# Optimization experiments

Hardware: AMD Instinct MI355X
Metric: run time of the kernel (lower is better)

## Reference

```python
import jax, jax.numpy as jnp
import numpy as np

HID = 2048
NKH, NVH = 16, 32
DK, DV = 128, 128
KCONV = 4
KEY_DIM = NKH * DK          # 2048
VAL_DIM = NVH * DV          # 4096
CONV_DIM = 2 * KEY_DIM + VAL_DIM  # 8192
QKVZ_DIM = 2 * KEY_DIM + 2 * VAL_DIM  # 12288
R = NVH // NKH              # 2
BA_DIM = 2 * NVH            # 64
EPS = 1e-6


def _l2norm(x, eps=1e-6):
    return x * jax.lax.rsqrt(jnp.sum(x * x, axis=-1, keepdims=True) + eps)


def setup_inputs() -> dict:
    key = jax.random.key(0)
    ks = jax.random.split(key, 8)
    std = 0.02
    return {
        "hidden_states": jax.random.normal(ks[0], (2, 2048, HID), dtype=jnp.float32),
        "attention_mask": jnp.ones((2, 2048), dtype=jnp.float32),
        "W_qkvz": jax.random.normal(ks[1], (HID, QKVZ_DIM), dtype=jnp.float32) * std,
        "W_ba": jax.random.normal(ks[2], (HID, BA_DIM), dtype=jnp.float32) * std,
        "conv_kernel": jax.random.normal(ks[3], (KCONV, 1, CONV_DIM), dtype=jnp.float32) * 0.1,
        "A_log": jnp.log(jax.random.uniform(ks[4], (NVH,), dtype=jnp.float32, minval=1.0, maxval=16.0)),
        "dt_bias": jnp.ones((NVH,), dtype=jnp.float32),
        "norm_kernel": jnp.ones((DV,), dtype=jnp.float32),
        "W_out": jax.random.normal(ks[5], (VAL_DIM, HID), dtype=jnp.float32) * std,
    }


def reference(hidden_states, attention_mask, W_qkvz, W_ba, conv_kernel, A_log, dt_bias, norm_kernel, W_out):
    b, s, _ = hidden_states.shape
    h = hidden_states * attention_mask[:, :, None]  # apply padding mask

    # projections
    qkvz = h @ W_qkvz  # (b, s, QKVZ_DIM)
    ba = h @ W_ba      # (b, s, BA_DIM)

    # fix_query_key_value_ordering: grouped per-k-head layout [q, k, v*R, z*R]
    qkvz = qkvz.reshape(b, s, NKH, 2 * DK + 2 * R * DV)
    q = qkvz[..., :DK]                                   # (b,s,NKH,DK)
    k = qkvz[..., DK:2 * DK]                             # (b,s,NKH,DK)
    v = qkvz[..., 2 * DK:2 * DK + R * DV].reshape(b, s, NVH, DV)
    z = qkvz[..., 2 * DK + R * DV:].reshape(b, s, NVH, DV)
    ba = ba.reshape(b, s, NKH, 2 * R)
    beta = ba[..., :R].reshape(b, s, NVH)
    alpha = ba[..., R:].reshape(b, s, NVH)

    # causal depthwise conv over [q|k|v] channels
    conv_in = jnp.concatenate(
        [q.reshape(b, s, -1), k.reshape(b, s, -1), v.reshape(b, s, -1)], axis=-1)  # (b,s,CONV_DIM)
    conv_out = jax.lax.conv_general_dilated(
        conv_in, conv_kernel, window_strides=(1,), padding=((KCONV - 1, 0),),
        dimension_numbers=("NWC", "WIO", "NWC"), feature_group_count=CONV_DIM)
    conv_out = jax.nn.silu(conv_out)

    q = conv_out[..., :KEY_DIM].reshape(b, s, NKH, DK)
    k = conv_out[..., KEY_DIM:2 * KEY_DIM].reshape(b, s, NKH, DK)
    v = conv_out[..., 2 * KEY_DIM:].reshape(b, s, NVH, DV)

    # expand k-heads to v-heads (repeat_interleave)
    q = jnp.repeat(q, R, axis=2)  # (b,s,NVH,DK)
    k = jnp.repeat(k, R, axis=2)

    # gated delta rule parameters
    g = -jnp.exp(A_log)[None, None, :] * jax.nn.softplus(alpha + dt_bias[None, None, :])  # (b,s,NVH)
    beta = jax.nn.sigmoid(beta)
    q = _l2norm(q) * (DK ** -0.5)
    k = _l2norm(k)

    # recurrence: S_t = exp(g_t) * S_{t-1} + k_t (v_t - k_t^T S) beta_t ; o_t = q_t^T S_t
    def step(S, x):
        q_t, k_t, v_t, g_t, b_t = x
        S = S * jnp.exp(g_t)[..., None, None]               # (b,h,DK,DV)
        kv = jnp.einsum("bhk,bhkv->bhv", k_t, S)
        delta = (v_t - kv) * b_t[..., None]
        S = S + jnp.einsum("bhk,bhv->bhkv", k_t, delta)
        o_t = jnp.einsum("bhk,bhkv->bhv", q_t, S)
        return S, o_t

    xs = (q.transpose(1, 0, 2, 3), k.transpose(1, 0, 2, 3), v.transpose(1, 0, 2, 3),
          g.transpose(1, 0, 2), beta.transpose(1, 0, 2))
    S0 = jnp.zeros((b, NVH, DK, DV), dtype=hidden_states.dtype)
    _, o = jax.lax.scan(step, S0, xs)
    o = o.transpose(1, 0, 2, 3)  # (b,s,NVH,DV)

    # gated RMSNorm per head (fp32 math as in Qwen3NextRMSNormGated)
    of = o.astype(jnp.float32)
    var = jnp.mean(of * of, axis=-1, keepdims=True)
    of = of * jax.lax.rsqrt(var + EPS)
    of = norm_kernel * of
    of = of * jax.nn.silu(z.astype(jnp.float32))
    o = of.astype(o.dtype).reshape(b, s, VAL_DIM)

    return o @ W_out
```

## Files before the change

kernel.cpp:

```cpp
#include <hip/hip_runtime.h>
#include <stdint.h>

typedef float    f32x4 __attribute__((ext_vector_type(4)));
typedef float    f32x2 __attribute__((ext_vector_type(2)));
typedef _Float16 f16x8 __attribute__((ext_vector_type(8)));
typedef _Float16 f16x4 __attribute__((ext_vector_type(4)));
typedef _Float16 f16x2 __attribute__((ext_vector_type(2)));

#define SEQ   2048
#define HIDD  2048
#define MROWS 4096
#define NQKV  12288
#define NCHUNK 32
#define CLEN   64

__device__ __forceinline__ void gload_lds16(const void* g, void* l) {
  __builtin_amdgcn_global_load_lds((const __attribute__((address_space(1))) uint32_t*)g,
                                   (__attribute__((address_space(3))) uint32_t*)l, 16, 0, 0);
}
__device__ __forceinline__ int swz256(int row, int colb) { return row * 256 + (colb ^ ((row & 7) << 4)); }
__device__ __forceinline__ int swz128(int row, int colb) { return row * 128 + (colb ^ ((row & 7) << 4)); }

__global__ __launch_bounds__(256)
void amask_kernel(const float* __restrict__ h, const float* __restrict__ mask,
                  _Float16* __restrict__ A1) {
  int i = blockIdx.x * 256 + threadIdx.x;
  if (i >= MROWS * HIDD / 4) return;
  f32x4 x = ((const f32x4*)h)[i];
  float m = mask[(i * 4) >> 11];
  f16x4 r;
  r[0] = (_Float16)(x[0] * m); r[1] = (_Float16)(x[1] * m);
  r[2] = (_Float16)(x[2] * m); r[3] = (_Float16)(x[3] * m);
  *(f16x4*)(A1 + (size_t)i * 4) = r;
}

__global__ __launch_bounds__(256)
void transpose_f16(const float* __restrict__ in, _Float16* __restrict__ out,
                   int R, int C) {
  __shared__ float tile[64][65];
  int c0 = blockIdx.x * 64, r0 = blockIdx.y * 64;
  int tx = threadIdx.x & 63, ty = threadIdx.x >> 6;
  #pragma unroll
  for (int i = 0; i < 16; ++i) {
    int r = i * 4 + ty;
    tile[r][tx] = in[(size_t)(r0 + r) * C + c0 + tx];
  }
  __syncthreads();
  #pragma unroll
  for (int i = 0; i < 16; ++i) {
    int c = i * 4 + ty;
    out[(size_t)(c0 + c) * R + r0 + tx] = (_Float16)tile[tx][c];
  }
}

template <typename CT, int BM>
__global__ __launch_bounds__(512, 2)
void gemm2ph(const _Float16* __restrict__ A, const _Float16* __restrict__ Bt,
             CT* __restrict__ C, int M, int N, int K, int tiles_n) {
  constexpr int RF  = BM / 32;
  constexpr int AR  = BM / 8;
  constexpr int NA  = AR / 8;
  constexpr int STG = NA + 4;
  __shared__ __align__(16) _Float16 lsA[2][BM * 64];
  __shared__ __align__(16) _Float16 lsB[2][256 * 64];
  int bm = blockIdx.x / tiles_n, bn = blockIdx.x % tiles_n;
  int m0 = bm * BM, n0 = bn * 256;
  int tid = threadIdx.x;
  int w = tid >> 6, lane = tid & 63;
  int wm = w >> 2, wn = w & 3;
  int la = lane & 15, lk = lane >> 4;
  int sr = lane >> 3;
  int scb = ((lane & 7) << 4) ^ ((sr & 7) << 4);
  int nkt = K >> 6;
  f32x4 acc[RF][4] = {};

  auto stage = [&](int kt, int buf) {
    const char* ga = (const char*)(A  + (size_t)(m0 + w * AR) * K + kt * 64);
    const char* gb = (const char*)(Bt + (size_t)(n0 + w * 32) * K + kt * 64);
    #pragma unroll
    for (int i = 0; i < NA; ++i)
      gload_lds16(ga + (size_t)(i * 8 + sr) * (K * 2) + scb, &lsA[buf][(w * AR + i * 8) * 64]);
    #pragma unroll
    for (int i = 0; i < 4; ++i)
      gload_lds16(gb + (size_t)(i * 8 + sr) * (K * 2) + scb, &lsB[buf][(w * 32 + i * 8) * 64]);
  };

  stage(0, 0);
  if (nkt > 1) stage(1, 1);

  int cur = 0;
  for (int kt = 0; kt < nkt; ++kt) {
    if (kt < nkt - 1) asm volatile("s_waitcnt vmcnt(%0)" :: "i"(STG) : "memory");
    else              asm volatile("s_waitcnt vmcnt(0)" ::: "memory");
    __builtin_amdgcn_s_barrier();
    const char* cA = (const char*)&lsA[cur][0];
    const char* cB = (const char*)&lsB[cur][0];
    #pragma unroll
    for (int kw = 0; kw < 2; ++kw) {
      f16x8 af[RF], bf[4];
      #pragma unroll
      for (int f = 0; f < RF; ++f) {
        int row = wm * (BM / 2) + f * 16 + la;
        af[f] = *(const f16x8*)(cA + row * 128 + ((kw * 64 + lk * 16) ^ ((row & 7) << 4)));
      }
      #pragma unroll
      for (int j = 0; j < 4; ++j) {
        int row = wn * 64 + j * 16 + la;
        bf[j] = *(const f16x8*)(cB + row * 128 + ((kw * 64 + lk * 16) ^ ((row & 7) << 4)));
      }
      #pragma unroll
      for (int f = 0; f < RF; ++f)
        #pragma unroll
        for (int j = 0; j < 4; ++j)
          acc[f][j] = __builtin_amdgcn_mfma_f32_16x16x32_f16(af[f], bf[j], acc[f][j], 0, 0, 0);
    }
    __builtin_amdgcn_s_barrier();
    if (kt + 2 < nkt) stage(kt + 2, cur);
    cur ^= 1;
  }

  #pragma unroll
  for (int f = 0; f < RF; ++f)
    #pragma unroll
    for (int j = 0; j < 4; ++j) {
      int col = n0 + wn * 64 + j * 16 + la;
      #pragma unroll
      for (int r = 0; r < 4; ++r) {
        int row = m0 + wm * (BM / 2) + f * 16 + lk * 4 + r;
        C[(size_t)row * N + col] = (CT)acc[f][j][r];
      }
    }
}

__global__ __launch_bounds__(256)
void ba_gemm(const float* __restrict__ h, const float* __restrict__ mask,
             const float* __restrict__ Wba, float* __restrict__ ba) {
  __shared__ float red[4][8][64];
  int r0 = blockIdx.x * 8;
  int c = threadIdx.x & 63, kc = threadIdx.x >> 6;
  float acc[8] = {};
  const float* wp = Wba + (size_t)(kc * 512) * 64 + c;
  const float* hp = h + (size_t)r0 * HIDD + kc * 512;
  for (int i = 0; i < 512; ++i) {
    float w = wp[(size_t)i * 64];
    #pragma unroll
    for (int r = 0; r < 8; ++r)
      acc[r] += hp[(size_t)r * HIDD + i] * w;
  }
  #pragma unroll
  for (int r = 0; r < 8; ++r) red[kc][r][c] = acc[r];
  __syncthreads();
  if (kc == 0) {
    #pragma unroll
    for (int r = 0; r < 8; ++r) {
      float s = red[0][r][c] + red[1][r][c] + red[2][r][c] + red[3][r][c];
      ba[(size_t)(r0 + r) * 64 + c] = s * mask[r0 + r];
    }
  }
}

__global__ __launch_bounds__(256)
void conv_kernel(const _Float16* __restrict__ qkvz, const float* __restrict__ ck,
                 _Float16* __restrict__ qn, _Float16* __restrict__ kn,
                 _Float16* __restrict__ vb) {
  int row = blockIdx.x;
  int b = row >> 11, t = row & 2047;
  int lane = threadIdx.x & 63, wid = threadIdx.x >> 6;
  for (int u = wid; u < 64; u += 4) {
    int c, cc, hh;
    if (u < 16)      { hh = u;      c = hh * 768;                               cc = hh * 128; }
    else if (u < 32) { hh = u - 16; c = hh * 768 + 128;                         cc = 2048 + hh * 128; }
    else             { hh = u - 32; c = (hh >> 1) * 768 + 256 + (hh & 1) * 128; cc = 4096 + hh * 128; }
    float y0 = 0.f, y1 = 0.f;
    #pragma unroll
    for (int j = 0; j < 4; ++j) {
      int tt = t - 3 + j;
      if (tt >= 0) {
        const _Float16* r = qkvz + (size_t)(b * 2048 + tt) * NQKV + c;
        f16x2 x = *(const f16x2*)(r + 2 * lane);
        f32x2 w = *(const f32x2*)(ck + j * 8192 + cc + 2 * lane);
        y0 += (float)x[0] * w[0];
        y1 += (float)x[1] * w[1];
      }
    }
    y0 = y0 / (1.f + expf(-y0));
    y1 = y1 / (1.f + expf(-y1));
    if (u < 32) {
      float ss = y0 * y0 + y1 * y1;
      #pragma unroll
      for (int m = 1; m < 64; m <<= 1) ss += __shfl_xor(ss, m);
      float rs = rsqrtf(ss + 1e-6f);
      if (u < 16) rs *= 0.08838834764831845f;
      y0 *= rs; y1 *= rs;
      _Float16* dst = (u < 16 ? qn : kn) + (size_t)row * 2048 + hh * 128;
      f16x2 o; o[0] = (_Float16)y0; o[1] = (_Float16)y1;
      *(f16x2*)(dst + 2 * lane) = o;
    } else {
      _Float16* dst = vb + (size_t)row * 4096 + hh * 128;
      f16x2 o; o[0] = (_Float16)y0; o[1] = (_Float16)y1;
      *(f16x2*)(dst + 2 * lane) = o;
    }
  }
}

__global__ __launch_bounds__(256)
void egbeta_kernel(const float* __restrict__ ba, const float* __restrict__ Alog,
                   const float* __restrict__ dtb, float* __restrict__ gout,
                   float* __restrict__ bout) {
  int i = blockIdx.x * 256 + threadIdx.x;
  if (i >= MROWS * 32) return;
  int vh = i >> 12, row = i & 4095;
  int kh = vh >> 1, r = vh & 1;
  const float* p = ba + (size_t)row * 64 + kh * 4;
  float bv = p[r], av = p[2 + r];
  float x = av + dtb[vh];
  float sp = (x > 20.f) ? x : log1pf(expf(x));
  gout[(size_t)vh * MROWS + row] = -expf(Alog[vh]) * sp;
  bout[(size_t)vh * MROWS + row] = 1.f / (1.f + expf(-bv));
}

__global__ __launch_bounds__(512, 2)
void chunk_scan(const _Float16* __restrict__ qn, const _Float16* __restrict__ kn,
                _Float16* __restrict__ vb, const float* __restrict__ gb,
                const float* __restrict__ btb) {
  __shared__ __align__(16) _Float16 Ks[64 * 128];
  __shared__ __align__(16) _Float16 Qs[64 * 128];
  __shared__ __align__(16) _Float16 Kt[128 * 64];
  __shared__ __align__(16) _Float16 Sf[32 * 128];
  __shared__ float AT[64 * 65];
  __shared__ __align__(16) _Float16 M16[64 * 64];
  __shared__ float RHS[32 * 65];
  __shared__ __align__(16) _Float16 Uv[32 * 64];
  __shared__ __align__(16) _Float16 Ub[32 * 64];
  __shared__ __align__(16) _Float16 Vb[64 * 32];
  __shared__ float gs[64], bs[64], cgs[64], bexp[64], scU[64];

  char* Ksb = (char*)Ks; char* Qsb = (char*)Qs; char* Ktb = (char*)Kt;
  char* Sfb = (char*)Sf; char* M16b = (char*)M16;
  char* Uvb = (char*)Uv; char* Ubb = (char*)Ub; char* Vbb = (char*)Vb;

  int bid = blockIdx.x;
  int b = bid >> 7, vh = (bid >> 2) & 31, vsl = bid & 3;
  int kh = vh >> 1;
  int tid = threadIdx.x;
  int w = tid >> 6, lane = tid & 63;
  int wr = w >> 1, wc = w & 1;
  int la = lane & 15, lk = lane >> 4;

  const _Float16* kgb = kn + (size_t)(b * 2048) * 2048 + kh * 128;
  const _Float16* qgb = qn + (size_t)(b * 2048) * 2048 + kh * 128;
  _Float16*       vgb = vb + (size_t)(b * 2048) * 4096 + vh * 128 + vsl * 32;
  const float*    ggb = gb  + (size_t)vh * MROWS + b * 2048;
  const float*    bgb = btb + (size_t)vh * MROWS + b * 2048;

  int srow = tid >> 3, sseg = tid & 7;
  int tk = tid & 127, tth = tid >> 7;

  f16x8 kr[2], qr[2]; f16x4 vr; float ebr;
  float sreg[2][4] = {};

  { f32x4 z = {}; ((f32x4*)Sf)[tid] = z; }

  kr[0] = *(const f16x8*)(kgb + (size_t)srow * 2048 + sseg * 16);
  kr[1] = *(const f16x8*)(kgb + (size_t)srow * 2048 + sseg * 16 + 8);
  qr[0] = *(const f16x8*)(qgb + (size_t)srow * 2048 + sseg * 16);
  qr[1] = *(const f16x8*)(qgb + (size_t)srow * 2048 + sseg * 16 + 8);
  vr    = *(const f16x4*)(vgb + (size_t)srow * 4096 + sseg * 4);
  ebr   = (tid < 64) ? ggb[tid] : (tid < 128 ? bgb[tid - 64] : 0.f);
  *(f16x8*)(Ksb + swz256(srow, sseg * 32))      = kr[0];
  *(f16x8*)(Ksb + swz256(srow, sseg * 32 + 16)) = kr[1];
  *(f16x8*)(Qsb + swz256(srow, sseg * 32))      = qr[0];
  *(f16x8*)(Qsb + swz256(srow, sseg * 32 + 16)) = qr[1];
  *(f16x4*)(Vbb + srow * 64 + sseg * 8) = vr;
  if (tid < 64) gs[tid] = ebr; else if (tid < 128) bs[tid - 64] = ebr;
  __syncthreads();

  #pragma unroll 1
  for (int c = 0; c < NCHUNK; ++c) {
    int cn = (c < NCHUNK - 1) ? c + 1 : c;
    kr[0] = *(const f16x8*)(kgb + (size_t)(cn * 64 + srow) * 2048 + sseg * 16);
    kr[1] = *(const f16x8*)(kgb + (size_t)(cn * 64 + srow) * 2048 + sseg * 16 + 8);
    qr[0] = *(const f16x8*)(qgb + (size_t)(cn * 64 + srow) * 2048 + sseg * 16);
    qr[1] = *(const f16x8*)(qgb + (size_t)(cn * 64 + srow) * 2048 + sseg * 16 + 8);
    vr    = *(const f16x4*)(vgb + (size_t)(cn * 64 + srow) * 4096 + sseg * 4);
    ebr   = (tid < 64) ? ggb[cn * 64 + tid] : (tid < 128 ? bgb[cn * 64 + tid - 64] : 0.f);

    f32x4 kk[2] = {}, qk[2] = {}, ks0 = {}, qs0 = {};
    #pragma unroll
    for (int ks = 0; ks < 4; ++ks) {
      f16x8 aK = *(const f16x8*)(Ksb + swz256(wr * 16 + la, ks * 64 + lk * 16));
      f16x8 aQ = *(const f16x8*)(Qsb + swz256(wr * 16 + la, ks * 64 + lk * 16));
      f16x8 bS = *(const f16x8*)(Sfb + swz256(wc * 16 + la, ks * 64 + lk * 16));
      #pragma unroll
      for (int j = 0; j < 2; ++j) {
        f16x8 bK = *(const f16x8*)(Ksb + swz256(wc * 32 + j * 16 + la, ks * 64 + lk * 16));
        kk[j] = __builtin_amdgcn_mfma_f32_16x16x32_f16(aK, bK, kk[j], 0, 0, 0);
        qk[j] = __builtin_amdgcn_mfma_f32_16x16x32_f16(aQ, bK, qk[j], 0, 0, 0);
      }
      ks0 = __builtin_amdgcn_mfma_f32_16x16x32_f16(aK, bS, ks0, 0, 0, 0);
      qs0 = __builtin_amdgcn_mfma_f32_16x16x32_f16(aQ, bS, qs0, 0, 0, 0);
    }
    {
      f16x8 r0, r1;
      #pragma unroll
      for (int j = 0; j < 8; ++j) {
        r0[j] = *(const _Float16*)(Ksb + swz256(tth * 16 + j, 2 * tk));
        r1[j] = *(const _Float16*)(Ksb + swz256(tth * 16 + 8 + j, 2 * tk));
      }
      *(f16x8*)(Ktb + swz128(tk, tth * 32))      = r0;
      *(f16x8*)(Ktb + swz128(tk, tth * 32 + 16)) = r1;
    }
    if (w == 0) {
      float g = gs[lane];
      #pragma unroll
      for (int off = 1; off < 64; off <<= 1) {
        float y = __shfl_up(g, off);
        if (lane >= off) g += y;
      }
      cgs[lane] = g;
      float cgL = __shfl(g, 63);
      bexp[lane] = __expf(g);
      scU[lane] = bs[lane] * __expf(cgL - g);
    }
    __syncthreads();

    {
      float cgt[4];
      #pragma unroll
      for (int r = 0; r < 4; ++r) cgt[r] = cgs[wr * 16 + lk * 4 + r];
      #pragma unroll
      for (int j = 0; j < 2; ++j) {
        int s = wc * 32 + j * 16 + la;
        float bsv = bs[s], cgss = cgs[s];
        #pragma unroll
        for (int r = 0; r < 4; ++r) {
          int t = wr * 16 + lk * 4 + r;
          float e = bsv * __expf(cgt[r] - cgss);
          AT[s * 65 + t] = (s < t) ? e * kk[j][r] : 0.f;
          float mm = (s <= t) ? e * qk[j][r] : 0.f;
          *(_Float16*)(M16b + swz128(t, s * 2)) = (_Float16)mm;
        }
      }
      #pragma unroll
      for (int r = 0; r < 4; ++r) {
        int t = wr * 16 + lk * 4 + r;
        int v = wc * 16 + la;
        float be = bexp[t];
        qs0[r] *= be;
        float vv = (float)*(const _Float16*)(Vbb + t * 64 + v * 2);
        RHS[v * 65 + t] = vv - be * ks0[r];
      }
    }
    __syncthreads();

    {
      float u[4];
      #pragma unroll
      for (int vi = 0; vi < 4; ++vi) u[vi] = RHS[(w * 4 + vi) * 65 + lane];
      #pragma unroll 1
      for (int sb = 0; sb < 8; ++sb) {
        float Ac[8];
        #pragma unroll
        for (int j = 0; j < 8; ++j) Ac[j] = AT[(sb * 8 + j) * 65 + lane];
        #pragma unroll
        for (int j = 0; j < 8; ++j) {
          int s = sb * 8 + j;
          #pragma unroll
          for (int vi = 0; vi < 4; ++vi) {
            float ubv = __builtin_bit_cast(float,
                __builtin_amdgcn_readlane(__builtin_bit_cast(int, u[vi]), s));
            u[vi] = fmaf(-Ac[j], ubv, u[vi]);
          }
        }
      }
      float sc = scU[lane];
      #pragma unroll
      for (int vi = 0; vi < 4; ++vi) {
        int v = w * 4 + vi;
        *(_Float16*)(Uvb + swz128(v, lane * 2)) = (_Float16)u[vi];
        *(_Float16*)(Ubb + swz128(v, lane * 2)) = (_Float16)(u[vi] * sc);
      }
    }
    __syncthreads();

    #pragma unroll
    for (int ss = 0; ss < 2; ++ss) {
      f16x8 aM = *(const f16x8*)(M16b + swz128(wr * 16 + la, ss * 64 + lk * 16));
      f16x8 bU = *(const f16x8*)(Uvb + swz128(wc * 16 + la, ss * 64 + lk * 16));
      qs0 = __builtin_amdgcn_mfma_f32_16x16x32_f16(aM, bU, qs0, 0, 0, 0);
    }
    #pragma unroll
    for (int r = 0; r < 4; ++r) {
      int t = wr * 16 + lk * 4 + r;
      vgb[(size_t)(c * 64 + t) * 4096 + wc * 16 + la] = (_Float16)qs0[r];
    }
    {
      f32x4 sd[2] = {};
      #pragma unroll
      for (int ss = 0; ss < 2; ++ss) {
        f16x8 bK = *(const f16x8*)(Ktb + swz128(w * 16 + la, ss * 64 + lk * 16));
        #pragma unroll
        for (int vt = 0; vt < 2; ++vt) {
          f16x8 aU = *(const f16x8*)(Ubb + swz128(vt * 16 + la, ss * 64 + lk * 16));
          sd[vt] = __builtin_amdgcn_mfma_f32_16x16x32_f16(aU, bK, sd[vt], 0, 0, 0);
        }
      }
      float beC = bexp[63];
      #pragma unroll
      for (int vt = 0; vt < 2; ++vt)
        #pragma unroll
        for (int r = 0; r < 4; ++r) {
          int v = vt * 16 + lk * 4 + r;
          int k = w * 16 + la;
          float sn = fmaf(sreg[vt][r], beC, sd[vt][r]);
          sreg[vt][r] = sn;
          *(_Float16*)(Sfb + swz256(v, k * 2)) = (_Float16)sn;
        }
    }
    __syncthreads();

    *(f16x8*)(Ksb + swz256(srow, sseg * 32))      = kr[0];
    *(f16x8*)(Ksb + swz256(srow, sseg * 32 + 16)) = kr[1];
    *(f16x8*)(Qsb + swz256(srow, sseg * 32))      = qr[0];
    *(f16x8*)(Qsb + swz256(srow, sseg * 32 + 16)) = qr[1];
    *(f16x4*)(Vbb + srow * 64 + sseg * 8) = vr;
    if (tid < 64) gs[tid] = ebr; else if (tid < 128) bs[tid - 64] = ebr;
    __syncthreads();
  }
}

__global__ __launch_bounds__(256)
void gate_kernel(const _Float16* __restrict__ ob, const _Float16* __restrict__ qkvz,
                 const float* __restrict__ nk, _Float16* __restrict__ Ag) {
  int row = blockIdx.x;
  int lane = threadIdx.x & 63, wid = threadIdx.x >> 6;
  for (int vh = wid; vh < 32; vh += 4) {
    const _Float16* op = ob + (size_t)row * 4096 + vh * 128;
    f16x2 xx = *(const f16x2*)(op + 2 * lane);
    float x0 = (float)xx[0], x1 = (float)xx[1];
    float ss = x0 * x0 + x1 * x1;
    #pragma unroll
    for (int m = 1; m < 64; m <<= 1) ss += __shfl_xor(ss, m);
    float rs = rsqrtf(ss * (1.f / 128.f) + 1e-6f);
    f32x2 nv = *(const f32x2*)(nk + 2 * lane);
    float v0 = x0 * rs * nv[0], v1 = x1 * rs * nv[1];
    const _Float16* zp = qkvz + (size_t)row * NQKV + (vh >> 1) * 768 + 512 + (vh & 1) * 128;
    f16x2 zz = *(const f16x2*)(zp + 2 * lane);
    float z0 = (float)zz[0], z1 = (float)zz[1];
    v0 *= z0 / (1.f + expf(-z0));
    v1 *= z1 / (1.f + expf(-z1));
    _Float16* dst = Ag + (size_t)row * 4096 + vh * 128;
    f16x2 o; o[0] = (_Float16)v0; o[1] = (_Float16)v1;
    *(f16x2*)(dst + 2 * lane) = o;
  }
}

extern "C" void kernel_launch(void* const* d_in, const int* in_sizes, int n_in,
                              void* d_out, int out_size, void* d_ws, size_t ws_size,
                              hipStream_t stream) {
  const float* h     = (const float*)d_in[0];
  const float* mask  = (const float*)d_in[1];
  const float* Wqkvz = (const float*)d_in[2];
  const float* Wba   = (const float*)d_in[3];
  const float* ck    = (const float*)d_in[4];
  const float* Alog  = (const float*)d_in[5];
  const float* dtb   = (const float*)d_in[6];
  const float* nk    = (const float*)d_in[7];
  const float* Wout  = (const float*)d_in[8];
  float* out = (float*)d_out;

  char* w = (char*)d_ws;
  const size_t o_qkvz = 0;
  const size_t o_A1   = 100663296;
  const size_t o_Bt1  = o_A1 + 16777216;
  const size_t o_ba   = o_Bt1 + 50331648;
  const size_t o_g    = o_ba + 1048576;
  const size_t o_bt   = o_g + 524288;
  const size_t total  = o_bt + 524288;
  if (ws_size < total) return;

  _Float16* qkvz16 = (_Float16*)(w + o_qkvz);
  _Float16* A1     = (_Float16*)(w + o_A1);
  _Float16* Bt1    = (_Float16*)(w + o_Bt1);
  float*    ba32   = (float*)   (w + o_ba);
  float*    gbuf   = (float*)   (w + o_g);
  float*    btb    = (float*)   (w + o_bt);
  _Float16* qn16 = (_Float16*)(w + o_A1);
  _Float16* kn16 = (_Float16*)(w + o_Bt1);
  _Float16* vb16 = (_Float16*)(w + o_Bt1 + 16777216);
  _Float16* Ag   = (_Float16*)(w + o_A1);
  _Float16* Wt2  = (_Float16*)(w + 0);

  amask_kernel<<<MROWS * HIDD / 4 / 256, 256, 0, stream>>>(h, mask, A1);
  transpose_f16<<<dim3(192, 32), 256, 0, stream>>>(Wqkvz, Bt1, HIDD, NQKV);
  ba_gemm<<<MROWS / 8, 256, 0, stream>>>(h, mask, Wba, ba32);
  gemm2ph<_Float16, 256><<<16 * 48, 512, 0, stream>>>(A1, Bt1, qkvz16, MROWS, NQKV, HIDD, 48);
  conv_kernel<<<MROWS, 256, 0, stream>>>(qkvz16, ck, qn16, kn16, vb16);
  egbeta_kernel<<<MROWS * 32 / 256, 256, 0, stream>>>(ba32, Alog, dtb, gbuf, btb);
  chunk_scan<<<256, 512, 0, stream>>>(qn16, kn16, vb16, gbuf, btb);
  gate_kernel<<<MROWS, 256, 0, stream>>>(vb16, qkvz16, nk, Ag);
  transpose_f16<<<dim3(32, 64), 256, 0, stream>>>(Wout, Wt2, 4096, HIDD);
  gemm2ph<float, 128><<<32 * 8, 512, 0, stream>>>(Ag, Wt2, out, MROWS, HIDD, 4096, 8);
}
```

Measured before the change: 700.2 us.

## Restructure GEMM main loop into barrier-separated phases with priority-boosted MFMA bursts

The GEMM k-loop now has a single-stage-ahead prefetch instead of prefetching two tiles. Each iteration loads B fragments and half of the A fragments into registers, then issues the next tile's global-to-LDS load. It runs four MFMA sub-phases separated by workgroup barriers, using s_setprio to raise priority during MFMA bursts and sched_barrier to pin instruction order. The intent is to overlap global loads with MFMA work and to interleave the two co-resident waves on each SIMD, in the style of 8-wave ping-pong schedules. The cost is many more barriers per iteration and a full vmcnt(0) wait at the top of every iteration, which could expose load latency.

```diff
diff --git a/kernel.cpp b/kernel.cpp
--- a/kernel.cpp
+++ b/kernel.cpp
@@ -55,12 +55,12 @@
 
 template <typename CT, int BM>
 __global__ __launch_bounds__(512, 2)
-void gemm2ph(const _Float16* __restrict__ A, const _Float16* __restrict__ Bt,
-             CT* __restrict__ C, int M, int N, int K, int tiles_n) {
+void gemm8p(const _Float16* __restrict__ A, const _Float16* __restrict__ Bt,
+            CT* __restrict__ C, int M, int N, int K, int tiles_n) {
   constexpr int RF  = BM / 32;
+  constexpr int RH  = RF / 2;
   constexpr int AR  = BM / 8;
   constexpr int NA  = AR / 8;
-  constexpr int STG = NA + 4;
   __shared__ __align__(16) _Float16 lsA[2][BM * 64];
   __shared__ __align__(16) _Float16 lsB[2][256 * 64];
   int bm = blockIdx.x / tiles_n, bn = blockIdx.x % tiles_n;
@@ -86,36 +86,85 @@
   };
 
   stage(0, 0);
-  if (nkt > 1) stage(1, 1);
 
   int cur = 0;
   for (int kt = 0; kt < nkt; ++kt) {
-    if (kt < nkt - 1) asm volatile("s_waitcnt vmcnt(%0)" :: "i"(STG) : "memory");
-    else              asm volatile("s_waitcnt vmcnt(0)" ::: "memory");
-    __builtin_amdgcn_s_barrier();
+    asm volatile("s_waitcnt vmcnt(0)" ::: "memory");
+    __builtin_amdgcn_s_barrier();
+    __builtin_amdgcn_sched_barrier(0);
     const char* cA = (const char*)&lsA[cur][0];
     const char* cB = (const char*)&lsB[cur][0];
-    #pragma unroll
-    for (int kw = 0; kw < 2; ++kw) {
-      f16x8 af[RF], bf[4];
-      #pragma unroll
-      for (int f = 0; f < RF; ++f) {
-        int row = wm * (BM / 2) + f * 16 + la;
-        af[f] = *(const f16x8*)(cA + row * 128 + ((kw * 64 + lk * 16) ^ ((row & 7) << 4)));
-      }
-      #pragma unroll
-      for (int j = 0; j < 4; ++j) {
+    f16x8 bf[4][2], af[RH][2];
+    #pragma unroll
+    for (int j = 0; j < 4; ++j)
+      #pragma unroll
+      for (int kw = 0; kw < 2; ++kw) {
         int row = wn * 64 + j * 16 + la;
-        bf[j] = *(const f16x8*)(cB + row * 128 + ((kw * 64 + lk * 16) ^ ((row & 7) << 4)));
-      }
-      #pragma unroll
-      for (int f = 0; f < RF; ++f)
-        #pragma unroll
-        for (int j = 0; j < 4; ++j)
-          acc[f][j] = __builtin_amdgcn_mfma_f32_16x16x32_f16(af[f], bf[j], acc[f][j], 0, 0, 0);
-    }
-    __builtin_amdgcn_s_barrier();
-    if (kt + 2 < nkt) stage(kt + 2, cur);
+        bf[j][kw] = *(const f16x8*)(cB + row * 128 + ((kw * 64 + lk * 16) ^ ((row & 7) << 4)));
+      }
+    #pragma unroll
+    for (int r = 0; r < RH; ++r)
+      #pragma unroll
+      for (int kw = 0; kw < 2; ++kw) {
+        int row = wm * (BM / 2) + r * 16 + la;
+        af[r][kw] = *(const f16x8*)(cA + row * 128 + ((kw * 64 + lk * 16) ^ ((row & 7) << 4)));
+      }
+    if (kt + 1 < nkt) stage(kt + 1, cur ^ 1);
+    __builtin_amdgcn_s_barrier();
+    __builtin_amdgcn_sched_barrier(0);
+    __builtin_amdgcn_s_setprio(1);
+    #pragma unroll
+    for (int r = 0; r < RH; ++r)
+      #pragma unroll
+      for (int j = 0; j < 2; ++j)
+        #pragma unroll
+        for (int kw = 0; kw < 2; ++kw)
+          acc[r][j] = __builtin_amdgcn_mfma_f32_16x16x32_f16(af[r][kw], bf[j][kw], acc[r][j], 0, 0, 0);
+    __builtin_amdgcn_s_setprio(0);
+    __builtin_amdgcn_s_barrier();
+    __builtin_amdgcn_sched_barrier(0);
+    __builtin_amdgcn_s_setprio(1);
+    #pragma unroll
+    for (int r = 0; r < RH; ++r)
+      #pragma unroll
+      for (int j = 2; j < 4; ++j)
+        #pragma unroll
+        for (int kw = 0; kw < 2; ++kw)
+          acc[r][j] = __builtin_amdgcn_mfma_f32_16x16x32_f16(af[r][kw], bf[j][kw], acc[r][j], 0, 0, 0);
+    __builtin_amdgcn_s_setprio(0);
+    __builtin_amdgcn_s_barrier();
+    __builtin_amdgcn_sched_barrier(0);
+    #pragma unroll
+    for (int r = 0; r < RH; ++r)
+      #pragma unroll
+      for (int kw = 0; kw < 2; ++kw) {
+        int row = wm * (BM / 2) + (RH + r) * 16 + la;
+        af[r][kw] = *(const f16x8*)(cA + row * 128 + ((kw * 64 + lk * 16) ^ ((row & 7) << 4)));
+      }
+    __builtin_amdgcn_s_barrier();
+    __builtin_amdgcn_sched_barrier(0);
+    __builtin_amdgcn_s_setprio(1);
+    #pragma unroll
+    for (int r = 0; r < RH; ++r)
+      #pragma unroll
+      for (int j = 0; j < 2; ++j)
+        #pragma unroll
+        for (int kw = 0; kw < 2; ++kw)
+          acc[RH + r][j] = __builtin_amdgcn_mfma_f32_16x16x32_f16(af[r][kw], bf[j][kw], acc[RH + r][j], 0, 0, 0);
+    __builtin_amdgcn_s_setprio(0);
+    __builtin_amdgcn_s_barrier();
+    __builtin_amdgcn_sched_barrier(0);
+    __builtin_amdgcn_s_setprio(1);
+    #pragma unroll
+    for (int r = 0; r < RH; ++r)
+      #pragma unroll
+      for (int j = 2; j < 4; ++j)
+        #pragma unroll
+        for (int kw = 0; kw < 2; ++kw)
+          acc[RH + r][j] = __builtin_amdgcn_mfma_f32_16x16x32_f16(af[r][kw], bf[j][kw], acc[RH + r][j], 0, 0, 0);
+    __builtin_amdgcn_s_setprio(0);
+    __builtin_amdgcn_s_barrier();
+    __builtin_amdgcn_sched_barrier(0);
     cur ^= 1;
   }
 
@@ -494,11 +543,11 @@
   amask_kernel<<<MROWS * HIDD / 4 / 256, 256, 0, stream>>>(h, mask, A1);
   transpose_f16<<<dim3(192, 32), 256, 0, stream>>>(Wqkvz, Bt1, HIDD, NQKV);
   ba_gemm<<<MROWS / 8, 256, 0, stream>>>(h, mask, Wba, ba32);
-  gemm2ph<_Float16, 256><<<16 * 48, 512, 0, stream>>>(A1, Bt1, qkvz16, MROWS, NQKV, HIDD, 48);
+  gemm8p<_Float16, 256><<<16 * 48, 512, 0, stream>>>(A1, Bt1, qkvz16, MROWS, NQKV, HIDD, 48);
   conv_kernel<<<MROWS, 256, 0, stream>>>(qkvz16, ck, qn16, kn16, vb16);
   egbeta_kernel<<<MROWS * 32 / 256, 256, 0, stream>>>(ba32, Alog, dtb, gbuf, btb);
   chunk_scan<<<256, 512, 0, stream>>>(qn16, kn16, vb16, gbuf, btb);
   gate_kernel<<<MROWS, 256, 0, stream>>>(vb16, qkvz16, nk, Ag);
   transpose_f16<<<dim3(32, 64), 256, 0, stream>>>(Wout, Wt2, 4096, HIDD);
-  gemm2ph<float, 128><<<32 * 8, 512, 0, stream>>>(Ag, Wt2, out, MROWS, HIDD, 4096, 8);
-}
+  gemm8p<float, 128><<<32 * 8, 512, 0, stream>>>(Ag, Wt2, out, MROWS, HIDD, 4096, 8);
+}
```

New measurement: 693.6 us. About the same (-0.9%).

## Restructure GEMM main loop into barrier-separated read/MFMA phases with XCD tile remap

Applied to the files above, without the earlier changes.

Replaces the two-stage prefetch GEMM loop with a one-ahead prefetch issued right after the first LDS reads. Each k-tile becomes alternating phases of LDS fragment reads and MFMA bursts, separated by workgroup barriers and sched_barriers, with raised wave priority during MFMA. Block indices are remapped so consecutive tiles land on the same XCD, aiming for better L2 reuse. The aim is to overlap LDS reads and global loads with matrix math across the two resident waves per SIMD. The trade-off is more barriers per k-tile and a shallower prefetch distance, with a full vmcnt(0) wait at the top of each iteration.

```diff
diff --git a/kernel.cpp b/kernel.cpp
--- a/kernel.cpp
+++ b/kernel.cpp
@@ -53,17 +53,20 @@
   }
 }
 
+#define SCHED0() __builtin_amdgcn_sched_barrier(0)
 template <typename CT, int BM>
 __global__ __launch_bounds__(512, 2)
-void gemm2ph(const _Float16* __restrict__ A, const _Float16* __restrict__ Bt,
-             CT* __restrict__ C, int M, int N, int K, int tiles_n) {
+void gemm4p(const _Float16* __restrict__ A, const _Float16* __restrict__ Bt,
+            CT* __restrict__ C, int M, int N, int K, int tiles_n) {
   constexpr int RF  = BM / 32;
+  constexpr int RH  = RF / 2;
   constexpr int AR  = BM / 8;
   constexpr int NA  = AR / 8;
-  constexpr int STG = NA + 4;
   __shared__ __align__(16) _Float16 lsA[2][BM * 64];
   __shared__ __align__(16) _Float16 lsB[2][256 * 64];
-  int bm = blockIdx.x / tiles_n, bn = blockIdx.x % tiles_n;
+  int cpx = gridDim.x >> 3;
+  int lid = (blockIdx.x & 7) * cpx + (blockIdx.x >> 3);
+  int bm = lid / tiles_n, bn = lid % tiles_n;
   int m0 = bm * BM, n0 = bn * 256;
   int tid = threadIdx.x;
   int w = tid >> 6, lane = tid & 63;
@@ -85,37 +88,49 @@
       gload_lds16(gb + (size_t)(i * 8 + sr) * (K * 2) + scb, &lsB[buf][(w * 32 + i * 8) * 64]);
   };
 
+#define READ_AF(dst, mh, kw)                                                       \
+  _Pragma("unroll") for (int r = 0; r < RH; ++r) {                                 \
+    int row_ = wm * (BM / 2) + ((mh) * RH + r) * 16 + la;                          \
+    dst[r] = *(const f16x8*)(cA + row_ * 128 + (((kw) * 64 + lk * 16) ^ ((row_ & 7) << 4))); }
+#define READ_BF(kw)                                                                \
+  _Pragma("unroll") for (int j = 0; j < 4; ++j) {                                  \
+    int row_ = wn * 64 + j * 16 + la;                                              \
+    bf[j] = *(const f16x8*)(cB + row_ * 128 + (((kw) * 64 + lk * 16) ^ ((row_ & 7) << 4))); }
+#define MFMA_PH(src, mh)                                                           \
+  __builtin_amdgcn_s_setprio(1);                                                   \
+  _Pragma("unroll") for (int r = 0; r < RH; ++r)                                   \
+    _Pragma("unroll") for (int j = 0; j < 4; ++j)                                  \
+      acc[(mh) * RH + r][j] =                                                      \
+        __builtin_amdgcn_mfma_f32_16x16x32_f16(src[r], bf[j], acc[(mh) * RH + r][j], 0, 0, 0); \
+  __builtin_amdgcn_s_setprio(0);
+
   stage(0, 0);
-  if (nkt > 1) stage(1, 1);
 
   int cur = 0;
   for (int kt = 0; kt < nkt; ++kt) {
-    if (kt < nkt - 1) asm volatile("s_waitcnt vmcnt(%0)" :: "i"(STG) : "memory");
-    else              asm volatile("s_waitcnt vmcnt(0)" ::: "memory");
+    asm volatile("s_waitcnt vmcnt(0)" ::: "memory");
     __builtin_amdgcn_s_barrier();
+    SCHED0();
     const char* cA = (const char*)&lsA[cur][0];
     const char* cB = (const char*)&lsB[cur][0];
-    #pragma unroll
-    for (int kw = 0; kw < 2; ++kw) {
-      f16x8 af[RF], bf[4];
-      #pragma unroll
-      for (int f = 0; f < RF; ++f) {
-        int row = wm * (BM / 2) + f * 16 + la;
-        af[f] = *(const f16x8*)(cA + row * 128 + ((kw * 64 + lk * 16) ^ ((row & 7) << 4)));
-      }
-      #pragma unroll
-      for (int j = 0; j < 4; ++j) {
-        int row = wn * 64 + j * 16 + la;
-        bf[j] = *(const f16x8*)(cB + row * 128 + ((kw * 64 + lk * 16) ^ ((row & 7) << 4)));
-      }
-      #pragma unroll
-      for (int f = 0; f < RF; ++f)
-        #pragma unroll
-        for (int j = 0; j < 4; ++j)
-          acc[f][j] = __builtin_amdgcn_mfma_f32_16x16x32_f16(af[f], bf[j], acc[f][j], 0, 0, 0);
-    }
-    __builtin_amdgcn_s_barrier();
-    if (kt + 2 < nkt) stage(kt + 2, cur);
+    f16x8 af0[RH], af1[RH], bf[4];
+    READ_BF(0); READ_AF(af0, 0, 0);
+    if (kt + 1 < nkt) stage(kt + 1, cur ^ 1);
+    SCHED0(); __builtin_amdgcn_s_barrier(); SCHED0();
+    MFMA_PH(af0, 0);
+    SCHED0(); __builtin_amdgcn_s_barrier(); SCHED0();
+    READ_AF(af1, 1, 0);
+    SCHED0(); __builtin_amdgcn_s_barrier(); SCHED0();
+    MFMA_PH(af1, 1);
+    SCHED0(); __builtin_amdgcn_s_barrier(); SCHED0();
+    READ_BF(1); READ_AF(af0, 0, 1);
+    SCHED0(); __builtin_amdgcn_s_barrier(); SCHED0();
+    MFMA_PH(af0, 0);
+    SCHED0(); __builtin_amdgcn_s_barrier(); SCHED0();
+    READ_AF(af1, 1, 1);
+    SCHED0(); __builtin_amdgcn_s_barrier(); SCHED0();
+    MFMA_PH(af1, 1);
+    SCHED0();
     cur ^= 1;
   }
 
@@ -130,6 +145,9 @@
         C[(size_t)row * N + col] = (CT)acc[f][j][r];
       }
     }
+#undef READ_AF
+#undef READ_BF
+#undef MFMA_PH
 }
 
 __global__ __launch_bounds__(256)
@@ -494,11 +512,11 @@
   amask_kernel<<<MROWS * HIDD / 4 / 256, 256, 0, stream>>>(h, mask, A1);
   transpose_f16<<<dim3(192, 32), 256, 0, stream>>>(Wqkvz, Bt1, HIDD, NQKV);
   ba_gemm<<<MROWS / 8, 256, 0, stream>>>(h, mask, Wba, ba32);
-  gemm2ph<_Float16, 256><<<16 * 48, 512, 0, stream>>>(A1, Bt1, qkvz16, MROWS, NQKV, HIDD, 48);
+  gemm4p<_Float16, 256><<<16 * 48, 512, 0, stream>>>(A1, Bt1, qkvz16, MROWS, NQKV, HIDD, 48);
   conv_kernel<<<MROWS, 256, 0, stream>>>(qkvz16, ck, qn16, kn16, vb16);
   egbeta_kernel<<<MROWS * 32 / 256, 256, 0, stream>>>(ba32, Alog, dtb, gbuf, btb);
   chunk_scan<<<256, 512, 0, stream>>>(qn16, kn16, vb16, gbuf, btb);
   gate_kernel<<<MROWS, 256, 0, stream>>>(vb16, qkvz16, nk, Ag);
   transpose_f16<<<dim3(32, 64), 256, 0, stream>>>(Wout, Wt2, 4096, HIDD);
-  gemm2ph<float, 128><<<32 * 8, 512, 0, stream>>>(Ag, Wt2, out, MROWS, HIDD, 4096, 8);
-}
+  gemm4p<float, 128><<<32 * 8, 512, 0, stream>>>(Ag, Wt2, out, MROWS, HIDD, 4096, 8);
+}
```

Measured after the change: 718.4 us. 1.03x slower.
